# Performance work log

Measured on AMD Instinct MI355X. Metric: run time of the kernel, lower is better.

## Reference

```python
import jax, jax.numpy as jnp
import numpy as np

B, T, N, DG = 4, 24, 2048, 64
E, H, W, P, NH = 128, 64, 64, 8, 4
HD = E // NH
HP, WP = H // P, W // P
NP = HP * WP
SCALE = float(np.sqrt(HD))


def _mlp(x, w1, b1, w2, b2):
    return jax.nn.relu(x @ w1 + b1) @ w2 + b2


def _interp_linear(x, out_len):
    # x: (B, L, C); linear interpolation along L to out_len, align_corners=False (PyTorch semantics)
    L = x.shape[1]
    src = jnp.maximum((jnp.arange(out_len, dtype=jnp.float32) + 0.5) * (L / out_len) - 0.5, 0.0)
    i0 = jnp.floor(src).astype(jnp.int32)
    lam = (src - i0.astype(jnp.float32))[None, :, None]
    i1 = jnp.minimum(i0 + 1, L - 1)
    return x[:, i0] * (1.0 - lam) + x[:, i1] * lam


def _cross_attn(Q, K, V, qw, qb, kw, kb, vw, vb, ow, ob):
    b, ql, _ = Q.shape
    kl = K.shape[1]
    q = (Q @ qw + qb).reshape(b, ql, NH, HD).transpose(0, 2, 1, 3)
    k = (K @ kw + kb).reshape(b, kl, NH, HD).transpose(0, 2, 1, 3)
    v = (V @ vw + vb).reshape(b, kl, NH, HD).transpose(0, 2, 1, 3)
    s = jnp.einsum('bhqd,bhkd->bhqk', q, k) / SCALE
    a = jax.nn.softmax(s, axis=-1)
    o = jnp.einsum('bhqk,bhkd->bhqd', a, v).transpose(0, 2, 1, 3).reshape(b, ql, E)
    o = o @ ow + ob
    # permute -> F.interpolate(size=k_len, mode='linear') -> permute back
    return _interp_linear(o, kl)


def _forward(graph_features, grid_features, graph_time_indices, grid_time_indices,
             gek_w1, gek_b1, gek_w2, gek_b2, gev_w1, gev_b1, gev_w2, gev_b2,
             rk_w1, rk_b1, rk_w2, rk_b2, rv_w1, rv_b1, rv_w2, rv_b2,
             te_w1, te_b1, te_w2, te_b2, pe_w, pe_b, up_w, up_b,
             ag_q_w, ag_q_b, ag_k_w, ag_k_b, ag_v_w, ag_v_b, ag_o_w, ag_o_b,
             ar_q_w, ar_q_b, ar_k_w, ar_k_b, ar_v_w, ar_v_b, ar_o_w, ar_o_b):
    # time embedding (query), q_len = T
    te = _mlp(graph_time_indices[:, :, None], te_w1, te_b1, te_w2, te_b2)  # (B, T, E)
    # graph branch
    gf = graph_features.reshape(B, T * N, DG)
    gk = _mlp(gf, gek_w1, gek_b1, gek_w2, gek_b2)
    gv = _mlp(gf, gev_w1, gev_b1, gev_w2, gev_b2)
    g_out = _cross_attn(te, gk, gv, ag_q_w, ag_q_b, ag_k_w, ag_k_b, ag_v_w, ag_v_b, ag_o_w, ag_o_b)
    g_out = g_out.reshape(B, T, N, E)
    # grid branch: non-overlapping patch conv (kernel=stride=P) as einsum
    xp = grid_features.reshape(B * T, E, HP, P, WP, P)
    patches = jnp.einsum('bchpwq,ocpq->bhwo', xp, pe_w) + pe_b  # (BT, HP, WP, E)
    patches = patches.reshape(B, T * NP, E)
    rk = _mlp(patches, rk_w1, rk_b1, rk_w2, rk_b2)
    rv = _mlp(patches, rv_w1, rv_b1, rv_w2, rv_b2)
    r_out = _cross_attn(te, rk, rv, ar_q_w, ar_q_b, ar_k_w, ar_k_b, ar_v_w, ar_v_b, ar_o_w, ar_o_b)  # (B, T*NP, E)
    r = r_out.reshape(B * T, HP, WP, E)
    # ConvTranspose2d with kernel=stride=P: each pixel expands to a PxP block
    up = jnp.einsum('bijc,copq->boipjq', r, up_w).reshape(B * T, E, H, W) + up_b[None, :, None, None]
    return g_out, up.reshape(B, T, E, H, W)


def setup_inputs():
    key = jax.random.key(0)
    ks = iter(jax.random.split(key, 64))
    def mk(shape):
        return jax.random.normal(next(ks), shape, dtype=jnp.float32) * 0.02
    d = {}
    d['graph_features'] = jax.random.normal(next(ks), (B, T, N, DG), dtype=jnp.float32)
    d['grid_features'] = jax.random.normal(next(ks), (B, T, E, H, W), dtype=jnp.float32)
    d['graph_time_indices'] = jax.random.uniform(next(ks), (B, T), dtype=jnp.float32)
    d['grid_time_indices'] = jax.random.uniform(next(ks), (B, T), dtype=jnp.float32)
    for pfx, din in (('gek', DG), ('gev', DG), ('rk', E), ('rv', E), ('te', 1)):
        d[pfx + '_w1'] = mk((din, E)); d[pfx + '_b1'] = jnp.zeros((E,), jnp.float32)
        d[pfx + '_w2'] = mk((E, E)); d[pfx + '_b2'] = jnp.zeros((E,), jnp.float32)
    d['pe_w'] = mk((E, E, P, P)); d['pe_b'] = jnp.zeros((E,), jnp.float32)
    d['up_w'] = mk((E, E, P, P)); d['up_b'] = jnp.zeros((E,), jnp.float32)
    for pfx in ('ag', 'ar'):
        for nm in ('q', 'k', 'v', 'o'):
            d[pfx + '_' + nm + '_w'] = mk((E, E)); d[pfx + '_' + nm + '_b'] = jnp.zeros((E,), jnp.float32)
    return d


def reference(graph_features, grid_features, graph_time_indices, grid_time_indices,
              gek_w1, gek_b1, gek_w2, gek_b2, gev_w1, gev_b1, gev_w2, gev_b2,
              rk_w1, rk_b1, rk_w2, rk_b2, rv_w1, rv_b1, rv_w2, rv_b2,
              te_w1, te_b1, te_w2, te_b2, pe_w, pe_b, up_w, up_b,
              ag_q_w, ag_q_b, ag_k_w, ag_k_b, ag_v_w, ag_v_b, ag_o_w, ag_o_b,
              ar_q_w, ar_q_b, ar_k_w, ar_k_b, ar_v_w, ar_v_b, ar_o_w, ar_o_b):
    return _forward(graph_features, grid_features, graph_time_indices, grid_time_indices,
                    gek_w1, gek_b1, gek_w2, gek_b2, gev_w1, gev_b1, gev_w2, gev_b2,
                    rk_w1, rk_b1, rk_w2, rk_b2, rv_w1, rv_b1, rv_w2, rv_b2,
                    te_w1, te_b1, te_w2, te_b2, pe_w, pe_b, up_w, up_b,
                    ag_q_w, ag_q_b, ag_k_w, ag_k_b, ag_v_w, ag_v_b, ag_o_w, ag_o_b,
                    ar_q_w, ar_q_b, ar_k_w, ar_k_b, ar_v_w, ar_v_b, ar_o_w, ar_o_b)
```

## Files before the change

### kernel.cpp

```cpp
#include <hip/hip_runtime.h>


typedef unsigned short u16;
using bf8 = __attribute__((ext_vector_type(8))) short;
using f4v = __attribute__((ext_vector_type(4))) float;
#define MFMA16(a, b, c) __builtin_amdgcn_mfma_f32_16x16x32_bf16(a, b, c, 0, 0, 0)

constexpr float INV_SCALE = 0.17677669529663687f;

__device__ __forceinline__ u16 f2bf(float f) {
  unsigned u = __float_as_uint(f);
  u += 0x7FFFu + ((u >> 16) & 1u);
  return (u16)(u >> 16);
}
__device__ __forceinline__ unsigned pk2(float a, float b) {
  return (unsigned)f2bf(a) | ((unsigned)f2bf(b) << 16);
}
__device__ __forceinline__ float bflo(unsigned v) { return __uint_as_float(v << 16); }
__device__ __forceinline__ float bfhi(unsigned v) { return __uint_as_float(v & 0xffff0000u); }


__global__ __launch_bounds__(128) void k_pre1(
    const float* gk_w1, const float* gv_w1, const float* rk_w1, const float* rv_w1,
    u16* W1c_g, u16* W1c_r,
    const float* pe_w, u16* peB,
    const float* tidx, const float* te_w1, const float* te_b1,
    const float* te_w2, const float* te_b2,
    const float* wg, const float* bg, const float* wr, const float* br,
    float* qg, float* qr,
    const float* A0, const float* Ab0, const float* B0, const float* Bb0, float* O0, float* Ob0,
    const float* A1, const float* Ab1, const float* B1, const float* Bb1, float* O1, float* Ob1,
    const float* A2, const float* Ab2, const float* B2, const float* Bb2, float* O2, float* Ob2,
    const float* A3, const float* Ab3, const float* B3, const float* Bb3, float* O3, float* Ob3) {
  int x = blockIdx.x, e = threadIdx.x;
  __shared__ float sh[256];
  if (x < 512) {
    int c = x & 255, brn = x >> 8;
    int DIN = brn ? 128 : 64;
    if (e < DIN) {
      const float* src = brn ? (c < 128 ? rk_w1 : rv_w1) : (c < 128 ? gk_w1 : gv_w1);
      u16* dst = brn ? W1c_r : W1c_g;
      dst[c * DIN + e] = f2bf(src[e * 128 + (c & 127)]);
    }
  } else if (x < 1536) {
    int i = ((x - 512) * 128 + e) * 8;
    float4 v0 = *(const float4*)(pe_w + i);
    float4 v1 = *(const float4*)(pe_w + i + 4);
    uint4 o; o.x = pk2(v0.x, v0.y); o.y = pk2(v0.z, v0.w);
    o.z = pk2(v1.x, v1.y); o.w = pk2(v1.z, v1.w);
    *(uint4*)&peB[i] = o;
  } else if (x < 1632) {
    int row = x - 1536;
    float tv = tidx[row];
    sh[e] = fmaxf(tv * te_w1[e] + te_b1[e], 0.f);
    __syncthreads();
    float a = te_b2[e];
    for (int j = 0; j < 128; ++j) a += sh[j] * te_w2[j * 128 + e];
    sh[128 + e] = a;
    __syncthreads();
    float ag = bg[e], ar = br[e];
    for (int j = 0; j < 128; ++j) {
      float xx = sh[128 + j];
      ag += xx * wg[j * 128 + e];
      ar += xx * wr[j * 128 + e];
    }
    qg[row * 128 + e] = ag;
    qr[row * 128 + e] = ar;
  } else {
    int sub = x - 1632;
    int task = sub / 129, j = sub % 129;
    const float *A, *Ab, *Bm, *Bb; float *O, *Ob;
    switch (task) {
      case 0: A=A0; Ab=Ab0; Bm=B0; Bb=Bb0; O=O0; Ob=Ob0; break;
      case 1: A=A1; Ab=Ab1; Bm=B1; Bb=Bb1; O=O1; Ob=Ob1; break;
      case 2: A=A2; Ab=Ab2; Bm=B2; Bb=Bb2; O=O2; Ob=Ob2; break;
      default:A=A3; Ab=Ab3; Bm=B3; Bb=Bb3; O=O3; Ob=Ob3; break;
    }
    sh[e] = (j < 128) ? A[j * 128 + e] : Ab[e];
    __syncthreads();
    float acc = (j < 128) ? 0.f : Bb[e];
    for (int m = 0; m < 128; ++m) acc += sh[m] * Bm[m * 128 + e];
    if (j < 128) O[j * 128 + e] = acc; else Ob[e] = acc;
  }
}


__global__ __launch_bounds__(128) void k_wvopk(
    const float* Wv_g, const float* bv_g, const float* ow_g, const float* ob_g, float* Wvo_g, float* bvo_g,
    const float* Wv_r, const float* bv_r, const float* ow_r, const float* ob_r, float* Wvo_r, float* bvo_r,
    const float* Wk_g, const float* bk_g, const float* q_g, u16* PkT_g, float* ck_g,
    const float* Wk_r, const float* bk_r, const float* q_r, u16* PkT_r, float* ck_r) {
  int j = blockIdx.x, e = threadIdx.x;
  if (blockIdx.y < 8) {
    int br = blockIdx.y >> 2, h = blockIdx.y & 3;
    const float* Wv = br ? Wv_r : Wv_g;  const float* bv = br ? bv_r : bv_g;
    const float* ow = br ? ow_r : ow_g;  const float* ob = br ? ob_r : ob_g;
    float* Wvo = br ? Wvo_r : Wvo_g;     float* bvo = br ? bvo_r : bvo_g;
    if (j < 128) {
      __shared__ float wrow[32];
      if (e < 32) wrow[e] = Wv[j * 128 + h * 32 + e];
      __syncthreads();
      float acc = 0.f;
      for (int d = 0; d < 32; ++d) acc += wrow[d] * ow[(h * 32 + d) * 128 + e];
      Wvo[(h * 128 + j) * 128 + e] = acc;
    } else if (h == 0) {
      __shared__ float bbv[128];
      bbv[e] = bv[e];
      __syncthreads();
      float acc = ob[e];
      for (int m = 0; m < 128; ++m) acc += bbv[m] * ow[m * 128 + e];
      bvo[e] = acc;
    }
  } else {
    int y = blockIdx.y - 8;
    int br = y >> 2, b = y & 3;
    int hq = e;
    if (hq >= 96) return;
    const float* Wk = br ? Wk_r : Wk_g;  const float* bk = br ? bk_r : bk_g;
    const float* q  = br ? q_r  : q_g;
    u16* PkT = br ? PkT_r : PkT_g;       float* ck = br ? ck_r : ck_g;
    int h = hq / 24, t = hq % 24;
    const float* qrow = q + (b * 24 + t) * 128 + h * 32;
    if (j < 128) {
      const float* wrow = Wk + j * 128 + h * 32;
      float acc = 0.f;
      for (int d = 0; d < 32; ++d) acc += wrow[d] * qrow[d];
      PkT[((size_t)b * 96 + hq) * 136 + j] = f2bf(acc * INV_SCALE);
    } else {
      float acc = 0.f;
      for (int d = 0; d < 32; ++d) acc += bk[h * 32 + d] * qrow[d];
      ck[b * 96 + hq] = acc * INV_SCALE;
    }
  }
}


template <int DIN, int NRED, bool INBF>
__device__ __forceinline__ void flash_body(char* smem,
    const void* __restrict__ Xv, const float* __restrict__ redbias, size_t rstride,
    const u16* __restrict__ W1c, const float* __restrict__ b1k, const float* __restrict__ b1v,
    const u16* __restrict__ PkT, const float* __restrict__ ck,
    u16* __restrict__ accP, float* __restrict__ lP,
    int KL, int kpb, int chunk, int b, int nchunk) {
  constexpr int KS = DIN / 32;
  constexpr int PD = DIN + 8;
  constexpr int PH = 136, PV = 72, PP = 72;
  constexpr int NR = DIN / 16;
  constexpr int XTN = 64 * PD;
  u16* Xt   = (u16*)smem;
  u16* HB   = (u16*)(smem + 4 * XTN);
  u16* Pt   = (u16*)(smem + 4 * XTN + 18432);
  u16* Pk_s = (u16*)(smem + 4 * XTN + 18432 + 13824);
  float* lred = (float*)(smem + 4 * XTN + 18432 + 13824 + 26112);

  int t = threadIdx.x;
  int l = t & 63, w = t >> 6;
  int l16 = l & 15, l4 = l >> 4;

  size_t xbase = (size_t)b * KL * DIN + (size_t)chunk * kpb * DIN;

  {
    const unsigned* ps = (const unsigned*)(PkT + (size_t)b * 96 * 136);
    unsigned* pd = (unsigned*)Pk_s;
    for (int i = t; i < 96 * 136 / 2; i += 256) pd[i] = ps[i];
  }

  bf8 wkA[2][KS], wvB[2][KS];
#pragma unroll
  for (int m = 0; m < 2; ++m)
#pragma unroll
    for (int ks = 0; ks < KS; ++ks) {
      int hid = w * 32 + m * 16 + l16;
      wkA[m][ks] = *(const bf8*)(W1c + (size_t)hid * DIN + ks * 32 + l4 * 8);
      wvB[m][ks] = *(const bf8*)(W1c + (size_t)(128 + hid) * DIN + ks * 32 + l4 * 8);
    }
  float bkA[2][4], bvB[2], ckr[6];
#pragma unroll
  for (int m = 0; m < 2; ++m)
#pragma unroll
    for (int r = 0; r < 4; ++r) bkA[m][r] = b1k[w * 32 + m * 16 + l4 * 4 + r];
#pragma unroll
  for (int n = 0; n < 2; ++n) bvB[n] = b1v[w * 32 + n * 16 + l16];
#pragma unroll
  for (int n = 0; n < 6; ++n) ckr[n] = ck[b * 96 + n * 16 + l16];

  f4v accO[6][2];
#pragma unroll
  for (int m = 0; m < 6; ++m)
#pragma unroll
    for (int n = 0; n < 2; ++n) accO[m][n] = (f4v){0.f, 0.f, 0.f, 0.f};
  float lacc[6] = {0.f, 0.f, 0.f, 0.f, 0.f, 0.f};

  float4 xr[NR];
  auto load_tile = [&](int kt) {
#pragma unroll
    for (int r = 0; r < NR; ++r) {
      int idx = (r * 256 + t) * 4;
      if constexpr (!INBF) {
        const float* Xrow = (const float*)Xv + xbase + (size_t)kt * 64 * DIN;
        xr[r] = *(const float4*)(Xrow + idx);
      } else {
        const u16* Xrow = (const u16*)Xv + xbase + (size_t)kt * 64 * DIN;
        int din = idx % DIN;
        float4 a = *(const float4*)(redbias + din);
#pragma unroll
        for (int c = 0; c < NRED; ++c) {
          uint2 v = *(const uint2*)(Xrow + (size_t)c * rstride + idx);
          a.x += bflo(v.x); a.y += bfhi(v.x);
          a.z += bflo(v.y); a.w += bfhi(v.y);
        }
        xr[r] = a;
      }
    }
  };

  int ntile = kpb >> 6;
  load_tile(0);
  int buf = 0;
  for (int kt = 0; kt < ntile; ++kt) {
#pragma unroll
    for (int r = 0; r < NR; ++r) {
      int idx = (r * 256 + t) * 4;
      int key = idx / DIN, din = idx % DIN;
      uint2 o; o.x = pk2(xr[r].x, xr[r].y); o.y = pk2(xr[r].z, xr[r].w);
      *(uint2*)&Xt[buf * XTN + key * PD + din] = o;
    }
    if (kt + 1 < ntile) load_tile(kt + 1);
    __syncthreads();

    {
      f4v hk[2][4];
#pragma unroll
      for (int m = 0; m < 2; ++m)
#pragma unroll
        for (int n = 0; n < 4; ++n) hk[m][n] = (f4v){0.f, 0.f, 0.f, 0.f};
#pragma unroll
      for (int ks = 0; ks < KS; ++ks) {
        bf8 xf[4];
#pragma unroll
        for (int n = 0; n < 4; ++n)
          xf[n] = *(const bf8*)&Xt[buf * XTN + (n * 16 + l16) * PD + ks * 32 + l4 * 8];
#pragma unroll
        for (int m = 0; m < 2; ++m)
#pragma unroll
          for (int n = 0; n < 4; ++n) hk[m][n] = MFMA16(wkA[m][ks], xf[n], hk[m][n]);
      }
#pragma unroll
      for (int m = 0; m < 2; ++m)
#pragma unroll
        for (int n = 0; n < 4; ++n) {
          int key = n * 16 + l16;
          int hid0 = w * 32 + m * 16 + l4 * 4;
          float v0 = fmaxf(hk[m][n][0] + bkA[m][0], 0.f);
          float v1 = fmaxf(hk[m][n][1] + bkA[m][1], 0.f);
          float v2 = fmaxf(hk[m][n][2] + bkA[m][2], 0.f);
          float v3 = fmaxf(hk[m][n][3] + bkA[m][3], 0.f);
          uint2 o; o.x = pk2(v0, v1); o.y = pk2(v2, v3);
          *(uint2*)&HB[key * PH + hid0] = o;
        }
    }
    __syncthreads();

    {
      f4v sa[6];
#pragma unroll
      for (int n = 0; n < 6; ++n) sa[n] = (f4v){ckr[n], ckr[n], ckr[n], ckr[n]};
#pragma unroll
      for (int ks = 0; ks < 4; ++ks) {
        bf8 a = *(const bf8*)&HB[(w * 16 + l16) * PH + ks * 32 + l4 * 8];
#pragma unroll
        for (int n = 0; n < 6; ++n) {
          bf8 bp = *(const bf8*)&Pk_s[(n * 16 + l16) * 136 + ks * 32 + l4 * 8];
          sa[n] = MFMA16(a, bp, sa[n]);
        }
      }
#pragma unroll
      for (int n = 0; n < 6; ++n) {
        float e0 = __expf(sa[n][0]), e1 = __expf(sa[n][1]);
        float e2 = __expf(sa[n][2]), e3 = __expf(sa[n][3]);
        float ls = (e0 + e1) + (e2 + e3);
        ls += __shfl_xor(ls, 16);
        ls += __shfl_xor(ls, 32);
        lacc[n] += ls;
        uint2 o; o.x = pk2(e0, e1); o.y = pk2(e2, e3);
        *(uint2*)&Pt[(n * 16 + l16) * PP + w * 16 + l4 * 4] = o;
      }
    }
    __syncthreads();

    {
      f4v hv[4][2];
#pragma unroll
      for (int m = 0; m < 4; ++m)
#pragma unroll
        for (int n = 0; n < 2; ++n) hv[m][n] = (f4v){0.f, 0.f, 0.f, 0.f};
#pragma unroll
      for (int ks = 0; ks < KS; ++ks) {
        bf8 xa[4];
#pragma unroll
        for (int m = 0; m < 4; ++m)
          xa[m] = *(const bf8*)&Xt[buf * XTN + (m * 16 + l16) * PD + ks * 32 + l4 * 8];
#pragma unroll
        for (int m = 0; m < 4; ++m)
#pragma unroll
          for (int n = 0; n < 2; ++n) hv[m][n] = MFMA16(xa[m], wvB[n][ks], hv[m][n]);
      }
#pragma unroll
      for (int m = 0; m < 4; ++m)
#pragma unroll
        for (int n = 0; n < 2; ++n) {
          int d = w * 32 + n * 16 + l16;
          int key0 = m * 16 + l4 * 4;
          float v0 = fmaxf(hv[m][n][0] + bvB[n], 0.f);
          float v1 = fmaxf(hv[m][n][1] + bvB[n], 0.f);
          float v2 = fmaxf(hv[m][n][2] + bvB[n], 0.f);
          float v3 = fmaxf(hv[m][n][3] + bvB[n], 0.f);
          uint2 o; o.x = pk2(v0, v1); o.y = pk2(v2, v3);
          *(uint2*)&HB[d * PV + key0] = o;
        }
    }

#pragma unroll
    for (int ks = 0; ks < 2; ++ks) {
      bf8 pa[6];
#pragma unroll
      for (int m = 0; m < 6; ++m)
        pa[m] = *(const bf8*)&Pt[(m * 16 + l16) * PP + ks * 32 + l4 * 8];
#pragma unroll
      for (int n = 0; n < 2; ++n) {
        bf8 hb = *(const bf8*)&HB[(w * 32 + n * 16 + l16) * PV + ks * 32 + l4 * 8];
#pragma unroll
        for (int m = 0; m < 6; ++m) accO[m][n] = MFMA16(pa[m], hb, accO[m][n]);
      }
    }
    buf ^= 1;
  }

  u16* ap = accP + (size_t)(b * nchunk + chunk) * 96 * 128;
#pragma unroll
  for (int m = 0; m < 6; ++m)
#pragma unroll
    for (int n = 0; n < 2; ++n) {
      int d = w * 32 + n * 16 + l16;
#pragma unroll
      for (int r = 0; r < 4; ++r) {
        int hq = m * 16 + l4 * 4 + r;
        ap[hq * 128 + d] = f2bf(accO[m][n][r]);
      }
    }
  if (l4 == 0) {
#pragma unroll
    for (int n = 0; n < 6; ++n) lred[w * 96 + n * 16 + l16] = lacc[n];
  }
  __syncthreads();
  if (t < 96) {
    float s = lred[t] + lred[96 + t] + lred[192 + t] + lred[288 + t];
    lP[(size_t)(b * nchunk + chunk) * 96 + t] = s;
  }
}


__device__ __forceinline__ void patch_body(char* smem, int bt, int kc,
    const float* __restrict__ X, const u16* __restrict__ peB,
    u16* __restrict__ patchP) {
  u16* Xp = (u16*)smem;
  u16* Wt = (u16*)(smem + 17408);
  int t = threadIdx.x;
  int l = t & 63, w = t >> 6;
  int l16 = l & 15, l4 = l >> 4;
  const float* Xbt = X + (size_t)bt * 524288 + (size_t)kc * 65536;

  f4v acc[4][2];
#pragma unroll
  for (int m = 0; m < 4; ++m)
#pragma unroll
    for (int n = 0; n < 2; ++n) acc[m][n] = (f4v){0.f, 0.f, 0.f, 0.f};

  float4 xr[8];
  auto loadX = [&](int s) {
    const float* img = Xbt + (size_t)s * 8192;
#pragma unroll
    for (int r = 0; r < 8; ++r) xr[r] = *(const float4*)(img + (r * 256 + t) * 4);
  };
  loadX(0);

  for (int s = 0; s < 8; ++s) {
#pragma unroll
    for (int r = 0; r < 8; ++r) {
      int idx = (r * 256 + t) * 4;
      int cl = idx >> 12, off = idx & 4095;
      int h = off >> 6, w0 = off & 63;
      int patch = (h >> 3) * 8 + (w0 >> 3);
      int within = (h & 7) * 8 + (w0 & 7);
      uint2 o; o.x = pk2(xr[r].x, xr[r].y); o.y = pk2(xr[r].z, xr[r].w);
      *(uint2*)&Xp[patch * 136 + cl * 64 + within] = o;
    }
    {
      int colbase = kc * 1024 + s * 128;
#pragma unroll
      for (int r = 0; r < 8; ++r) {
        int idx = r * 256 + t;
        int co = idx >> 4, part = idx & 15;
        int slot = part ^ (co & 7);
        uint4 v = *(const uint4*)(peB + (size_t)co * 8192 + colbase + part * 8);
        *(uint4*)&Wt[co * 128 + slot * 8] = v;
      }
    }
    if (s < 7) loadX(s + 1);
    __syncthreads();
#pragma unroll
    for (int ks2 = 0; ks2 < 4; ++ks2) {
      bf8 af[4];
#pragma unroll
      for (int m = 0; m < 4; ++m)
        af[m] = *(const bf8*)&Xp[(m * 16 + l16) * 136 + ks2 * 32 + l4 * 8];
#pragma unroll
      for (int n = 0; n < 2; ++n) {
        int co = w * 32 + n * 16 + l16;
        int slot = (ks2 * 4 + l4) ^ (co & 7);
        bf8 bf_ = *(const bf8*)&Wt[co * 128 + slot * 8];
#pragma unroll
        for (int m = 0; m < 4; ++m) acc[m][n] = MFMA16(af[m], bf_, acc[m][n]);
      }
    }
    __syncthreads();
  }
  u16* outp = patchP + ((size_t)kc * 6144 + bt * 64) * 128;
#pragma unroll
  for (int m = 0; m < 4; ++m)
#pragma unroll
    for (int n = 0; n < 2; ++n) {
      int d = w * 32 + n * 16 + l16;
#pragma unroll
      for (int r = 0; r < 4; ++r) {
        int patch = m * 16 + l4 * 4 + r;
        outp[patch * 128 + d] = f2bf(acc[m][n][r]);
      }
    }
}


__device__ __forceinline__ void ogred_body(char* smem, int t, int b, int nc,
    const u16* __restrict__ accP, const float* __restrict__ lP,
    const float* __restrict__ Wvo, const float* __restrict__ bvo,
    float* __restrict__ og) {
  float* part = (float*)smem;
  float* invl = part + 2048;
  float* red  = part + 2052;
  int tid = threadIdx.x;
  int oct = tid & 15, h = (tid >> 4) & 3, cq = tid >> 6;
  int cn = nc >> 2;
  float a8[8];
#pragma unroll
  for (int k = 0; k < 8; ++k) a8[k] = 0.f;
  const u16* base = accP + ((size_t)(b * nc + cq * cn) * 96 + h * 24 + t) * 128 + oct * 8;
  for (int c = 0; c < cn; ++c) {
    uint4 v = *(const uint4*)(base + (size_t)c * 12288);
    a8[0] += bflo(v.x); a8[1] += bfhi(v.x);
    a8[2] += bflo(v.y); a8[3] += bfhi(v.y);
    a8[4] += bflo(v.z); a8[5] += bfhi(v.z);
    a8[6] += bflo(v.w); a8[7] += bfhi(v.w);
  }
#pragma unroll
  for (int k = 0; k < 8; ++k) part[cq * 512 + h * 128 + oct * 8 + k] = a8[k];
  if (tid < 64) {
    int hh = tid >> 4, c0 = tid & 15;
    float ls = 0.f;
    for (int c = c0; c < nc; c += 16) ls += lP[(size_t)(b * nc + c) * 96 + hh * 24 + t];
    ls += __shfl_xor(ls, 8); ls += __shfl_xor(ls, 4);
    ls += __shfl_xor(ls, 2); ls += __shfl_xor(ls, 1);
    if (c0 == 0) invl[hh] = 1.f / ls;
  }
  __syncthreads();
  for (int p = tid; p < 512; p += 256) {
    float s = (part[p] + part[512 + p]) + (part[1024 + p] + part[1536 + p]);
    part[p] = s * invl[p >> 7];
  }
  __syncthreads();
  {
    int e = tid & 127, jh = tid >> 7;
    float acc = jh ? 0.f : bvo[e];
    for (int h2 = 0; h2 < 4; ++h2) {
      const float* wv = Wvo + (size_t)(h2 * 128 + jh * 64) * 128 + e;
      const float* o = part + h2 * 128 + jh * 64;
#pragma unroll 4
      for (int j = 0; j < 64; ++j) acc += o[j] * wv[(size_t)j * 128];
    }
    red[tid] = acc;
  }
  __syncthreads();
  if (tid < 128) og[(b * 24 + t) * 128 + tid] = red[tid] + red[128 + tid];
}


__global__ __launch_bounds__(256, 2) void k_big1(
    const float* __restrict__ gf, const u16* __restrict__ W1c_g,
    const float* __restrict__ gek_b1, const float* __restrict__ gev_b1,
    const u16* __restrict__ PkT_g, const float* __restrict__ ck_g,
    u16* __restrict__ accP_g, float* __restrict__ lP_g,
    const float* __restrict__ gridf, const u16* __restrict__ peB,
    u16* __restrict__ patchP) {
  __shared__ __align__(16) char smem[78336];
  int x = blockIdx.x;
  if (x < 128) {
    flash_body<64, 1, false>(smem, gf, (const float*)nullptr, 0,
        W1c_g, gek_b1, gev_b1, PkT_g, ck_g, accP_g, lP_g,
        49152, 1536, x & 31, x >> 5, 32);
  } else {
    int pid = x - 128;
    patch_body(smem, pid % 96, pid / 96, gridf, peB, patchP);
  }
}


__global__ __launch_bounds__(256, 2) void k_big2(
    const u16* __restrict__ accP_g, const float* __restrict__ lP_g,
    const float* __restrict__ Wvo_g, const float* __restrict__ bvo_g,
    float* __restrict__ og_g,
    const u16* __restrict__ patchP, const float* __restrict__ pe_b,
    const u16* __restrict__ W1c_r,
    const float* __restrict__ rk_b1, const float* __restrict__ rv_b1,
    const u16* __restrict__ PkT_r, const float* __restrict__ ck_r,
    u16* __restrict__ accP_r, float* __restrict__ lP_r) {
  __shared__ __align__(16) char smem[94720];
  int x = blockIdx.x;
  if (x < 96) {
    ogred_body(smem, x % 24, x / 24, 32, accP_g, lP_g, Wvo_g, bvo_g, og_g);
  } else {
    int fid = x - 96;
    flash_body<128, 8, true>(smem, patchP, pe_b, 786432,
        W1c_r, rk_b1, rv_b1, PkT_r, ck_r, accP_r, lP_r,
        1536, 192, fid & 7, fid >> 3, 8);
  }
}


__global__ __launch_bounds__(256) void k_big3(
    const u16* __restrict__ accP_r, const float* __restrict__ lP_r,
    const float* __restrict__ Wvo_r, const float* __restrict__ bvo_r,
    float* __restrict__ og_r,
    const float* __restrict__ og_g, float* __restrict__ outg) {
  __shared__ __align__(16) char smem[9232];
  int x = blockIdx.x;
  if (x < 96) {
    ogred_body(smem, x % 24, x / 24, 8, accP_r, lP_r, Wvo_r, bvo_r, og_r);
  } else {
    int vx = x - 96;
    int b = vx >> 10;
    const float* ogb = og_g + b * 3072;
    float* ob = outg + (size_t)b * 6291456;
    for (int i4 = (vx & 1023) * 256 + threadIdx.x; i4 < 1572864; i4 += 1024 * 256) {
      int i = i4 * 4;
      int n = i >> 7, e = i & 127;
      float src = fmaxf((n + 0.5f) * (1.f / 2048.f) - 0.5f, 0.f);
      int t0 = (int)src; float lam = src - (float)t0; int t1 = min(t0 + 1, 23);
      float4 a = *(const float4*)&ogb[t0 * 128 + e];
      float4 c = *(const float4*)&ogb[t1 * 128 + e];
      float4 o;
      o.x = a.x + lam * (c.x - a.x); o.y = a.y + lam * (c.y - a.y);
      o.z = a.z + lam * (c.z - a.z); o.w = a.w + lam * (c.w - a.w);
      *(float4*)&ob[i] = o;
    }
  }
}


__global__ __launch_bounds__(256) void k_upfuse(const float* __restrict__ og_r,
    const float* __restrict__ up_w, const float* __restrict__ up_b,
    float* __restrict__ outu) {
  int b = blockIdx.x >> 7, o = blockIdx.x & 127;
  __shared__ float og_s[24 * 128];
  __shared__ float upw_s[128 * 64];
  __shared__ float U_s[24 * 64];
  int tid = threadIdx.x;
  for (int i = tid; i < 24 * 128 / 4; i += 256)
    ((float4*)og_s)[i] = ((const float4*)(og_r + b * 3072))[i];
  for (int i = tid; i < 128 * 64 / 4; i += 256) {
    int c = i >> 4, pq4 = i & 15;
    ((float4*)upw_s)[i] = *(const float4*)(up_w + (size_t)c * 8192 + o * 64 + pq4 * 4);
  }
  __syncthreads();
  float bias = up_b[o];
  int pq = tid & 63, tg = tid >> 6;
  float acc[6] = {0.f, 0.f, 0.f, 0.f, 0.f, 0.f};
  for (int c = 0; c < 128; c += 4) {
    float w0 = upw_s[c * 64 + pq], w1 = upw_s[(c + 1) * 64 + pq];
    float w2 = upw_s[(c + 2) * 64 + pq], w3 = upw_s[(c + 3) * 64 + pq];
#pragma unroll
    for (int r = 0; r < 6; ++r) {
      float4 g = *(const float4*)&og_s[(tg * 6 + r) * 128 + c];
      acc[r] += g.x * w0 + g.y * w1 + g.z * w2 + g.w * w3;
    }
  }
#pragma unroll
  for (int r = 0; r < 6; ++r) U_s[(tg * 6 + r) * 64 + pq] = acc[r] + bias;
  __syncthreads();
  for (int i4 = tid; i4 < 24 * 1024; i4 += 256) {
    int i = i4 * 4;
    int t = i >> 12, hw = i & 4095;
    int h = hw >> 6, w0 = hw & 63;
    int ii = h >> 3, p = h & 7, j = w0 >> 3, q0 = w0 & 7;
    int n = t * 64 + ii * 8 + j;
    float src = fmaxf((n + 0.5f) * (1.f / 64.f) - 0.5f, 0.f);
    int t0 = (int)src; float lam = src - (float)t0; int t1 = min(t0 + 1, 23);
    float4 a = *(const float4*)&U_s[t0 * 64 + p * 8 + q0];
    float4 c4 = *(const float4*)&U_s[t1 * 64 + p * 8 + q0];
    float4 r;
    r.x = a.x + lam * (c4.x - a.x); r.y = a.y + lam * (c4.y - a.y);
    r.z = a.z + lam * (c4.z - a.z); r.w = a.w + lam * (c4.w - a.w);
    *(float4*)&outu[((size_t)(b * 24 + t) * 128 + o) * 4096 + hw] = r;
  }
}


extern "C" void kernel_launch(void* const* d_in, const int* in_sizes, int n_in,
                              void* d_out, int out_size, void* d_ws, size_t ws_size,
                              hipStream_t stream) {
  (void)in_sizes; (void)n_in; (void)out_size; (void)ws_size;
  const float* gf    = (const float*)d_in[0];
  const float* gridf = (const float*)d_in[1];
  const float* gti   = (const float*)d_in[2];
  const float* gek_w1 = (const float*)d_in[4],  *gek_b1 = (const float*)d_in[5];
  const float* gek_w2 = (const float*)d_in[6],  *gek_b2 = (const float*)d_in[7];
  const float* gev_w1 = (const float*)d_in[8],  *gev_b1 = (const float*)d_in[9];
  const float* gev_w2 = (const float*)d_in[10], *gev_b2 = (const float*)d_in[11];
  const float* rk_w1  = (const float*)d_in[12], *rk_b1  = (const float*)d_in[13];
  const float* rk_w2  = (const float*)d_in[14], *rk_b2  = (const float*)d_in[15];
  const float* rv_w1  = (const float*)d_in[16], *rv_b1  = (const float*)d_in[17];
  const float* rv_w2  = (const float*)d_in[18], *rv_b2  = (const float*)d_in[19];
  const float* te_w1  = (const float*)d_in[20], *te_b1  = (const float*)d_in[21];
  const float* te_w2  = (const float*)d_in[22], *te_b2  = (const float*)d_in[23];
  const float* pe_w   = (const float*)d_in[24], *pe_b   = (const float*)d_in[25];
  const float* up_w   = (const float*)d_in[26], *up_b   = (const float*)d_in[27];
  const float* ag_q_w = (const float*)d_in[28], *ag_q_b = (const float*)d_in[29];
  const float* ag_k_w = (const float*)d_in[30], *ag_k_b = (const float*)d_in[31];
  const float* ag_v_w = (const float*)d_in[32], *ag_v_b = (const float*)d_in[33];
  const float* ag_o_w = (const float*)d_in[34], *ag_o_b = (const float*)d_in[35];
  const float* ar_q_w = (const float*)d_in[36], *ar_q_b = (const float*)d_in[37];
  const float* ar_k_w = (const float*)d_in[38], *ar_k_b = (const float*)d_in[39];
  const float* ar_v_w = (const float*)d_in[40], *ar_v_b = (const float*)d_in[41];
  const float* ar_o_w = (const float*)d_in[42], *ar_o_b = (const float*)d_in[43];

  float* out = (float*)d_out;
  float* ws = (float*)d_ws;
  size_t off = 0;
  auto A = [&](size_t n) { float* p = ws + off; off += n; return p; };
  float* q_g   = A(12288);   float* q_r   = A(12288);
  float* Wk_g  = A(16384);   float* bk_g  = A(128);
  float* Wv_g  = A(16384);   float* bv_g  = A(128);
  float* Wk_r  = A(16384);   float* bk_r  = A(128);
  float* Wv_r  = A(16384);   float* bv_r  = A(128);
  float* Wvo_g = A(65536);   float* bvo_g = A(128);
  float* Wvo_r = A(65536);   float* bvo_r = A(128);
  float* ck_g  = A(384);     float* ck_r  = A(384);
  u16*   PkT_g = (u16*)A(26112);
  u16*   PkT_r = (u16*)A(26112);
  u16*   W1c_g = (u16*)A(8192);
  u16*   W1c_r = (u16*)A(16384);
  u16*   peB   = (u16*)A(524288);
  float* lP_g  = A(12288);   float* lP_r  = A(3072);
  float* og_g  = A(12288);   float* og_r  = A(12288);
  u16*   accP_g = (u16*)A(786432);
  u16*   patchP = (u16*)A(3145728);
  u16*   accP_r = (u16*)A(196608);

  k_pre1<<<2148, 128, 0, stream>>>(
      gek_w1, gev_w1, rk_w1, rv_w1, W1c_g, W1c_r,
      pe_w, peB,
      gti, te_w1, te_b1, te_w2, te_b2, ag_q_w, ag_q_b, ar_q_w, ar_q_b, q_g, q_r,
      gek_w2, gek_b2, ag_k_w, ag_k_b, Wk_g, bk_g,
      gev_w2, gev_b2, ag_v_w, ag_v_b, Wv_g, bv_g,
      rk_w2,  rk_b2,  ar_k_w, ar_k_b, Wk_r, bk_r,
      rv_w2,  rv_b2,  ar_v_w, ar_v_b, Wv_r, bv_r);
  k_wvopk<<<dim3(129, 16), 128, 0, stream>>>(
      Wv_g, bv_g, ag_o_w, ag_o_b, Wvo_g, bvo_g,
      Wv_r, bv_r, ar_o_w, ar_o_b, Wvo_r, bvo_r,
      Wk_g, bk_g, q_g, PkT_g, ck_g,
      Wk_r, bk_r, q_r, PkT_r, ck_r);

  k_big1<<<896, 256, 0, stream>>>(
      gf, W1c_g, gek_b1, gev_b1, PkT_g, ck_g, accP_g, lP_g,
      gridf, peB, patchP);
  k_big2<<<128, 256, 0, stream>>>(
      accP_g, lP_g, Wvo_g, bvo_g, og_g,
      patchP, pe_b, W1c_r, rk_b1, rv_b1, PkT_r, ck_r, accP_r, lP_r);
  k_big3<<<4192, 256, 0, stream>>>(
      accP_r, lP_r, Wvo_r, bvo_r, og_r, og_g, out);
  k_upfuse<<<512, 256, 0, stream>>>(og_r, up_w, up_b, out + 25165824);
}
```

Measured before the change: 206.2 us.

## Fuse four main kernels into a persistent megakernel with grid barriers

Replaces the k_big1/k_big2/k_big3/k_upfuse launches with one 512-block persistent kernel. Graph-branch and grid-branch blocks progress independently and are separated by atomic-counter grid barriers rather than kernel boundaries. The goal is to remove launch gaps and let the graph branch overlap with the grid branch. To fit within shared memory, the grid flash path drops double buffering in favour of a per-iteration syncthreads. This risks deadlock if not all 512 blocks are co-resident, and it cuts parallelism in phases where many blocks sit idle.

```diff
diff --git a/kernel.cpp b/kernel.cpp
--- a/kernel.cpp
+++ b/kernel.cpp
@@ -18,6 +18,24 @@
 }
 __device__ __forceinline__ float bflo(unsigned v) { return __uint_as_float(v << 16); }
 __device__ __forceinline__ float bfhi(unsigned v) { return __uint_as_float(v & 0xffff0000u); }
+
+__device__ __forceinline__ void gbar(unsigned* bs, int idx, unsigned nblk) {
+  __syncthreads();
+  if (threadIdx.x == 0) {
+    __threadfence();
+    unsigned v = __hip_atomic_fetch_add(bs + idx, 1u, __ATOMIC_ACQ_REL,
+                                        __HIP_MEMORY_SCOPE_AGENT);
+    if (v == nblk - 1) {
+      __hip_atomic_store(bs + 8 + idx, 1u, __ATOMIC_RELEASE,
+                         __HIP_MEMORY_SCOPE_AGENT);
+    } else {
+      while (!__hip_atomic_load(bs + 8 + idx, __ATOMIC_ACQUIRE,
+                                __HIP_MEMORY_SCOPE_AGENT))
+        __builtin_amdgcn_s_sleep(2);
+    }
+  }
+  __syncthreads();
+}
 
 
 __global__ __launch_bounds__(128) void k_pre1(
@@ -31,9 +49,11 @@
     const float* A0, const float* Ab0, const float* B0, const float* Bb0, float* O0, float* Ob0,
     const float* A1, const float* Ab1, const float* B1, const float* Bb1, float* O1, float* Ob1,
     const float* A2, const float* Ab2, const float* B2, const float* Bb2, float* O2, float* Ob2,
-    const float* A3, const float* Ab3, const float* B3, const float* Bb3, float* O3, float* Ob3) {
+    const float* A3, const float* Ab3, const float* B3, const float* Bb3, float* O3, float* Ob3,
+    unsigned* barstate) {
   int x = blockIdx.x, e = threadIdx.x;
   __shared__ float sh[256];
+  if (x == 0 && e < 16) barstate[e] = 0;
   if (x < 512) {
     int c = x & 255, brn = x >> 8;
     int DIN = brn ? 128 : 64;
@@ -135,7 +155,7 @@
 }
 
 
-template <int DIN, int NRED, bool INBF>
+template <int DIN, int NRED, bool INBF, bool DBUF>
 __device__ __forceinline__ void flash_body(char* smem,
     const void* __restrict__ Xv, const float* __restrict__ redbias, size_t rstride,
     const u16* __restrict__ W1c, const float* __restrict__ b1k, const float* __restrict__ b1v,
@@ -147,11 +167,12 @@
   constexpr int PH = 136, PV = 72, PP = 72;
   constexpr int NR = DIN / 16;
   constexpr int XTN = 64 * PD;
+  constexpr int XTB = (DBUF ? 2 : 1) * 2 * XTN;
   u16* Xt   = (u16*)smem;
-  u16* HB   = (u16*)(smem + 4 * XTN);
-  u16* Pt   = (u16*)(smem + 4 * XTN + 18432);
-  u16* Pk_s = (u16*)(smem + 4 * XTN + 18432 + 13824);
-  float* lred = (float*)(smem + 4 * XTN + 18432 + 13824 + 26112);
+  u16* HB   = (u16*)(smem + XTB);
+  u16* Pt   = (u16*)(smem + XTB + 18432);
+  u16* Pk_s = (u16*)(smem + XTB + 18432 + 13824);
+  float* lred = (float*)(smem + XTB + 18432 + 13824 + 26112);
 
   int t = threadIdx.x;
   int l = t & 63, w = t >> 6;
@@ -333,7 +354,8 @@
         for (int m = 0; m < 6; ++m) accO[m][n] = MFMA16(pa[m], hb, accO[m][n]);
       }
     }
-    buf ^= 1;
+    if constexpr (DBUF) buf ^= 1;
+    else __syncthreads();
   }
 
   u16* ap = accP + (size_t)(b * nchunk + chunk) * 96 * 128;
@@ -493,85 +515,12 @@
 }
 
 
-__global__ __launch_bounds__(256, 2) void k_big1(
-    const float* __restrict__ gf, const u16* __restrict__ W1c_g,
-    const float* __restrict__ gek_b1, const float* __restrict__ gev_b1,
-    const u16* __restrict__ PkT_g, const float* __restrict__ ck_g,
-    u16* __restrict__ accP_g, float* __restrict__ lP_g,
-    const float* __restrict__ gridf, const u16* __restrict__ peB,
-    u16* __restrict__ patchP) {
-  __shared__ __align__(16) char smem[78336];
-  int x = blockIdx.x;
-  if (x < 128) {
-    flash_body<64, 1, false>(smem, gf, (const float*)nullptr, 0,
-        W1c_g, gek_b1, gev_b1, PkT_g, ck_g, accP_g, lP_g,
-        49152, 1536, x & 31, x >> 5, 32);
-  } else {
-    int pid = x - 128;
-    patch_body(smem, pid % 96, pid / 96, gridf, peB, patchP);
-  }
-}
-
-
-__global__ __launch_bounds__(256, 2) void k_big2(
-    const u16* __restrict__ accP_g, const float* __restrict__ lP_g,
-    const float* __restrict__ Wvo_g, const float* __restrict__ bvo_g,
-    float* __restrict__ og_g,
-    const u16* __restrict__ patchP, const float* __restrict__ pe_b,
-    const u16* __restrict__ W1c_r,
-    const float* __restrict__ rk_b1, const float* __restrict__ rv_b1,
-    const u16* __restrict__ PkT_r, const float* __restrict__ ck_r,
-    u16* __restrict__ accP_r, float* __restrict__ lP_r) {
-  __shared__ __align__(16) char smem[94720];
-  int x = blockIdx.x;
-  if (x < 96) {
-    ogred_body(smem, x % 24, x / 24, 32, accP_g, lP_g, Wvo_g, bvo_g, og_g);
-  } else {
-    int fid = x - 96;
-    flash_body<128, 8, true>(smem, patchP, pe_b, 786432,
-        W1c_r, rk_b1, rv_b1, PkT_r, ck_r, accP_r, lP_r,
-        1536, 192, fid & 7, fid >> 3, 8);
-  }
-}
-
-
-__global__ __launch_bounds__(256) void k_big3(
-    const u16* __restrict__ accP_r, const float* __restrict__ lP_r,
-    const float* __restrict__ Wvo_r, const float* __restrict__ bvo_r,
-    float* __restrict__ og_r,
-    const float* __restrict__ og_g, float* __restrict__ outg) {
-  __shared__ __align__(16) char smem[9232];
-  int x = blockIdx.x;
-  if (x < 96) {
-    ogred_body(smem, x % 24, x / 24, 8, accP_r, lP_r, Wvo_r, bvo_r, og_r);
-  } else {
-    int vx = x - 96;
-    int b = vx >> 10;
-    const float* ogb = og_g + b * 3072;
-    float* ob = outg + (size_t)b * 6291456;
-    for (int i4 = (vx & 1023) * 256 + threadIdx.x; i4 < 1572864; i4 += 1024 * 256) {
-      int i = i4 * 4;
-      int n = i >> 7, e = i & 127;
-      float src = fmaxf((n + 0.5f) * (1.f / 2048.f) - 0.5f, 0.f);
-      int t0 = (int)src; float lam = src - (float)t0; int t1 = min(t0 + 1, 23);
-      float4 a = *(const float4*)&ogb[t0 * 128 + e];
-      float4 c = *(const float4*)&ogb[t1 * 128 + e];
-      float4 o;
-      o.x = a.x + lam * (c.x - a.x); o.y = a.y + lam * (c.y - a.y);
-      o.z = a.z + lam * (c.z - a.z); o.w = a.w + lam * (c.w - a.w);
-      *(float4*)&ob[i] = o;
-    }
-  }
-}
-
-
-__global__ __launch_bounds__(256) void k_upfuse(const float* __restrict__ og_r,
-    const float* __restrict__ up_w, const float* __restrict__ up_b,
-    float* __restrict__ outu) {
-  int b = blockIdx.x >> 7, o = blockIdx.x & 127;
-  __shared__ float og_s[24 * 128];
-  __shared__ float upw_s[128 * 64];
-  __shared__ float U_s[24 * 64];
+__device__ __forceinline__ void upfuse_body(char* smem, int b, int o,
+    const float* __restrict__ og_r, const float* __restrict__ up_w,
+    const float* __restrict__ up_b, float* __restrict__ outu) {
+  float* og_s  = (float*)smem;
+  float* upw_s = og_s + 3072;
+  float* U_s   = upw_s + 8192;
   int tid = threadIdx.x;
   for (int i = tid; i < 24 * 128 / 4; i += 256)
     ((float4*)og_s)[i] = ((const float4*)(og_r + b * 3072))[i];
@@ -609,6 +558,77 @@
     r.x = a.x + lam * (c4.x - a.x); r.y = a.y + lam * (c4.y - a.y);
     r.z = a.z + lam * (c4.z - a.z); r.w = a.w + lam * (c4.w - a.w);
     *(float4*)&outu[((size_t)(b * 24 + t) * 128 + o) * 4096 + hw] = r;
+  }
+}
+
+
+__global__ __launch_bounds__(256, 2) void k_mega(
+    const float* __restrict__ gf, const u16* __restrict__ W1c_g,
+    const float* __restrict__ gek_b1, const float* __restrict__ gev_b1,
+    const u16* __restrict__ PkT_g, const float* __restrict__ ck_g,
+    u16* __restrict__ accP_g, float* __restrict__ lP_g,
+    const float* __restrict__ Wvo_g, const float* __restrict__ bvo_g,
+    float* __restrict__ og_g,
+    const float* __restrict__ gridf, const u16* __restrict__ peB,
+    u16* __restrict__ patchP, const float* __restrict__ pe_b,
+    const u16* __restrict__ W1c_r,
+    const float* __restrict__ rk_b1, const float* __restrict__ rv_b1,
+    const u16* __restrict__ PkT_r, const float* __restrict__ ck_r,
+    u16* __restrict__ accP_r, float* __restrict__ lP_r,
+    const float* __restrict__ Wvo_r, const float* __restrict__ bvo_r,
+    float* __restrict__ og_r,
+    const float* __restrict__ up_w, const float* __restrict__ up_b,
+    float* __restrict__ outg, float* __restrict__ outu,
+    unsigned* __restrict__ barstate) {
+  __shared__ __align__(16) char smem[78336];
+  int x = blockIdx.x;
+  if (x < 128) {
+    flash_body<64, 1, false, true>(smem, gf, (const float*)nullptr, 0,
+        W1c_g, gek_b1, gev_b1, PkT_g, ck_g, accP_g, lP_g,
+        49152, 1536, x & 31, x >> 5, 32);
+    gbar(barstate, 0, 128);
+    if (x < 96)
+      ogred_body(smem, x % 24, x / 24, 32, accP_g, lP_g, Wvo_g, bvo_g, og_g);
+    gbar(barstate, 1, 128);
+    for (int b = 0; b < 4; ++b) {
+      const float* ogb = og_g + b * 3072;
+      float* ob = outg + (size_t)b * 6291456;
+      for (int i4 = x * 256 + threadIdx.x; i4 < 1572864; i4 += 128 * 256) {
+        int i = i4 * 4;
+        int n = i >> 7, e = i & 127;
+        float src = fmaxf((n + 0.5f) * (1.f / 2048.f) - 0.5f, 0.f);
+        int t0 = (int)src; float lam = src - (float)t0; int t1 = min(t0 + 1, 23);
+        float4 a = *(const float4*)&ogb[t0 * 128 + e];
+        float4 c = *(const float4*)&ogb[t1 * 128 + e];
+        float4 o;
+        o.x = a.x + lam * (c.x - a.x); o.y = a.y + lam * (c.y - a.y);
+        o.z = a.z + lam * (c.z - a.z); o.w = a.w + lam * (c.w - a.w);
+        *(float4*)&ob[i] = o;
+      }
+    }
+  } else {
+    int x2 = x - 128;
+    patch_body(smem, x2 % 96, x2 / 96, gridf, peB, patchP);
+    {
+      int u = x2 + 384;
+      patch_body(smem, u % 96, u / 96, gridf, peB, patchP);
+    }
+    gbar(barstate, 2, 384);
+    if (x2 < 32) {
+      flash_body<128, 8, true, false>(smem, patchP, pe_b, 786432,
+          W1c_r, rk_b1, rv_b1, PkT_r, ck_r, accP_r, lP_r,
+          1536, 192, x2 & 7, x2 >> 3, 8);
+    }
+    gbar(barstate, 3, 384);
+    if (x2 < 96)
+      ogred_body(smem, x2 % 24, x2 / 24, 8, accP_r, lP_r, Wvo_r, bvo_r, og_r);
+    gbar(barstate, 4, 384);
+    upfuse_body(smem, x2 >> 7, x2 & 127, og_r, up_w, up_b, outu);
+    if (x2 < 128) {
+      int u = x2 + 384;
+      __syncthreads();
+      upfuse_body(smem, u >> 7, u & 127, og_r, up_w, up_b, outu);
+    }
   }
 }
 
@@ -663,6 +683,7 @@
   u16*   accP_g = (u16*)A(786432);
   u16*   patchP = (u16*)A(3145728);
   u16*   accP_r = (u16*)A(196608);
+  unsigned* barstate = (unsigned*)A(16);
 
   k_pre1<<<2148, 128, 0, stream>>>(
       gek_w1, gev_w1, rk_w1, rv_w1, W1c_g, W1c_r,
@@ -671,20 +692,18 @@
       gek_w2, gek_b2, ag_k_w, ag_k_b, Wk_g, bk_g,
       gev_w2, gev_b2, ag_v_w, ag_v_b, Wv_g, bv_g,
       rk_w2,  rk_b2,  ar_k_w, ar_k_b, Wk_r, bk_r,
-      rv_w2,  rv_b2,  ar_v_w, ar_v_b, Wv_r, bv_r);
+      rv_w2,  rv_b2,  ar_v_w, ar_v_b, Wv_r, bv_r,
+      barstate);
   k_wvopk<<<dim3(129, 16), 128, 0, stream>>>(
       Wv_g, bv_g, ag_o_w, ag_o_b, Wvo_g, bvo_g,
       Wv_r, bv_r, ar_o_w, ar_o_b, Wvo_r, bvo_r,
       Wk_g, bk_g, q_g, PkT_g, ck_g,
       Wk_r, bk_r, q_r, PkT_r, ck_r);
 
-  k_big1<<<896, 256, 0, stream>>>(
+  k_mega<<<512, 256, 0, stream>>>(
       gf, W1c_g, gek_b1, gev_b1, PkT_g, ck_g, accP_g, lP_g,
-      gridf, peB, patchP);
-  k_big2<<<128, 256, 0, stream>>>(
-      accP_g, lP_g, Wvo_g, bvo_g, og_g,
-      patchP, pe_b, W1c_r, rk_b1, rv_b1, PkT_r, ck_r, accP_r, lP_r);
-  k_big3<<<4192, 256, 0, stream>>>(
-      accP_r, lP_r, Wvo_r, bvo_r, og_r, og_g, out);
-  k_upfuse<<<512, 256, 0, stream>>>(og_r, up_w, up_b, out + 25165824);
-}
+      Wvo_g, bvo_g, og_g,
+      gridf, peB, patchP, pe_b, W1c_r, rk_b1, rv_b1, PkT_r, ck_r,
+      accP_r, lP_r, Wvo_r, bvo_r, og_r,
+      up_w, up_b, out, out + 25165824, barstate);
+}
```

After: 726.7 us. 252% more time.
